# Performance work log

Measured on AMD Instinct MI355X. Metric: run time of the kernel, lower is better.

The kernel has to match this reference:

```python
import jax, jax.numpy as jnp
import numpy as np

N_WIRES = 12
BLOCK_CONFIGS = [(12, 3), (12, 3)]
HAM_OFFSET = 0.0
HAM_COEFF = 1.0
BATCH = 4096


def _sq(psi, w):
    # view statevector (B, 2^n) as (B, left, 2, right) isolating wire w
    B = psi.shape[0]
    n = N_WIRES
    return psi.reshape(B, 1 << w, 2, 1 << (n - 1 - w))


def _rx(psi, theta, w):
    s = _sq(psi, w)
    t = jnp.asarray(theta, jnp.float32).reshape(-1, 1, 1, 1) * 0.5
    out = jnp.cos(t) * s - 1j * jnp.sin(t) * jnp.flip(s, axis=2)
    return out.reshape(psi.shape)


def _ry(psi, theta, w):
    # [[c,-s],[s,c]]: new = cos*psi + sin*sgn*flip(psi), sgn = (-1, +1)
    s = _sq(psi, w)
    t = jnp.asarray(theta, jnp.float32).reshape(-1, 1, 1, 1) * 0.5
    sgn = jnp.array([-1.0, 1.0], jnp.float32).reshape(1, 1, 2, 1)
    out = jnp.cos(t) * s + jnp.sin(t) * sgn * jnp.flip(s, axis=2)
    return out.reshape(psi.shape)


def _rz(psi, theta, w):
    # diag(e^{-i t/2}, e^{+i t/2})
    s = _sq(psi, w)
    t = jnp.asarray(theta, jnp.float32).reshape(-1, 1, 1, 1) * 0.5
    z = jnp.array([-1.0, 1.0], jnp.float32).reshape(1, 1, 2, 1)
    out = s * jnp.exp(1j * (t * z).astype(jnp.complex64))
    return out.reshape(psi.shape)


def _cnot(psi, c, t):
    B = psi.shape[0]
    n = N_WIRES
    lo, hi = (c, t) if c < t else (t, c)
    s = psi.reshape(B, 1 << lo, 2, 1 << (hi - lo - 1), 2, 1 << (n - 1 - hi))
    ctrl_ax = 2 if c == lo else 4
    tgt_ax = 4 if c == lo else 2
    p0 = jax.lax.index_in_dim(s, 0, axis=ctrl_ax, keepdims=True)
    p1 = jnp.flip(jax.lax.index_in_dim(s, 1, axis=ctrl_ax, keepdims=True), axis=tgt_ax)
    out = jnp.concatenate([p0, p1], axis=ctrl_ax)
    return out.reshape(psi.shape)


def setup_inputs() -> dict:
    key = jax.random.key(0)
    k1, k2 = jax.random.split(key)
    total_encode = sum(ne for ne, _ in BLOCK_CONFIGS)
    total_ansatz = sum(ld for _, ld in BLOCK_CONFIGS)
    x = jax.random.normal(k1, (BATCH, total_encode), dtype=jnp.float32)
    ansatz_weights = jax.random.uniform(
        k2, (total_ansatz, 3, N_WIRES), dtype=jnp.float32,
        minval=-np.pi, maxval=np.pi)
    return {"x": x, "ansatz_weights": ansatz_weights}


def reference(x, ansatz_weights):
    B = x.shape[0]
    n = N_WIRES
    psi = jnp.zeros((B, 1 << n), jnp.complex64).at[:, 0].set(1.0)
    param_col = 0
    ansatz_block = 0
    for n_encode, linear_depth in BLOCK_CONFIGS:
        for j in range(n_encode):
            wire = j % n
            if param_col < x.shape[1]:
                psi = _rx(psi, x[:, param_col], wire)
            param_col += 1
        for _ in range(linear_depth):
            w = ansatz_weights[ansatz_block]
            for i in range(n):
                psi = _ry(psi, w[0, i], i)
                psi = _rz(psi, w[1, i], i)
                psi = _ry(psi, w[2, i], i)
            for i in range(n):
                psi = _cnot(psi, i, (i + 1) % n)
            ansatz_block += 1
    # <H> with H = offset + coeff * sum_i Z_i : diagonal = n - 2*popcount(k)
    probs = psi.real ** 2 + psi.imag ** 2
    k = jnp.arange(1 << n)
    pop = ((k[:, None] >> jnp.arange(n)[None, :]) & 1).sum(-1).astype(jnp.float32)
    diag = HAM_OFFSET + HAM_COEFF * (n - 2.0 * pop)
    expval = probs @ diag  # (B,)
    return expval[:, None]
```

## Files before the change

kernel.cpp:

```cpp
#include <hip/hip_runtime.h>
#include <math.h>

#define NTP 256
#define NT 64
#define NS 4096

typedef float f32x2 __attribute__((ext_vector_type(2)));

constexpr int ring_pi_c(int k) {
    int u = k ^ (k >> 1);
    u ^= u >> 2; u ^= u >> 4; u ^= u >> 8;
    int w0 = ((u >> 11) ^ u) & 1;
    return (u & 0x7FF) | (w0 << 11);
}
constexpr int gfun(int n) {
    int n0 = n & 1, n1 = (n >> 1) & 1, n2 = (n >> 2) & 1, n3 = (n >> 3) & 1;
    return (n1) | ((n0 ^ n1 ^ n2) << 1) | ((n0 ^ n2 ^ n3) << 2) | ((n0 ^ n3) << 3);
}
constexpr int sigf(int k) { return k ^ gfun((k >> 6) & 15); }

__device__ __forceinline__ void app1p(f32x2 ab, f32x2 cd, f32x2& a0, f32x2& a1) {
    f32x2 n0, n1;
    asm("v_pk_mul_f32 %0, %2, %4 op_sel:[0,0] op_sel_hi:[1,0]\n\t"
        "v_pk_fma_f32 %0, %2, %4, %0 op_sel:[1,1,0] op_sel_hi:[0,1,1] neg_hi:[0,1,0]\n\t"
        "v_pk_fma_f32 %0, %3, %5, %0 op_sel:[0,0,0] op_sel_hi:[1,0,1] neg_lo:[0,1,0] neg_hi:[0,1,0]\n\t"
        "v_pk_fma_f32 %0, %3, %5, %0 op_sel:[1,1,0] op_sel_hi:[0,1,1] neg_lo:[0,1,0]\n\t"
        "v_pk_mul_f32 %1, %3, %4 op_sel:[0,0] op_sel_hi:[1,0]\n\t"
        "v_pk_fma_f32 %1, %3, %4, %1 op_sel:[1,1,0] op_sel_hi:[0,1,1] neg_lo:[0,1,0]\n\t"
        "v_pk_fma_f32 %1, %2, %5, %1 op_sel:[0,0,0] op_sel_hi:[1,0,1]\n\t"
        "v_pk_fma_f32 %1, %2, %5, %1 op_sel:[1,1,0] op_sel_hi:[0,1,1] neg_lo:[0,1,0]"
        : "=&v"(n0), "=&v"(n1)
        : "v"(a0), "v"(a1), "v"(ab), "v"(cd));
    a0 = n0; a1 = n1;
}

template<int P>
__device__ __forceinline__ void gate_on_bit6(f32x2 a[64], f32x2 ab, f32x2 cd) {
    #pragma unroll
    for (int r = 0; r < 64; ++r)
        if (!(r & (1 << P)))
            app1p(ab, cd, a[r], a[r | (1 << P)]);
}

__device__ __forceinline__ void load_gate(const float4* __restrict__ Uw,
                                          const float2* __restrict__ cs12,
                                          int lay, int w, bool fold,
                                          f32x2& ab, f32x2& cd) {
    float4 g = Uw[lay * 12 + w];
    float A = g.x, B = g.y, C = g.z, D = g.w;
    if (fold) {
        float2 sc = cs12[w];
        float c = sc.x, s = sc.y;
        float A2 = A*c + D*s, B2 = B*c - C*s, C2 = C*c + B*s, D2 = D*c - A*s;
        A = A2; B = B2; C = C2; D = D2;
    }
    ab = f32x2{A, B}; cd = f32x2{C, D};
}

__global__ void prep_kernel(const float* __restrict__ x,
                            const float* __restrict__ wts,
                            float4* __restrict__ Uw,
                            float2* __restrict__ cs,
                            int total)
{
    int idx = blockIdx.x * blockDim.x + threadIdx.x;
    if (idx < total) {
        float th = 0.5f * x[idx];
        float s, c; sincosf(th, &s, &c);
        cs[idx] = make_float2(c, s);
    }
    if (idx < 72) {
        int ab = idx / 12, w = idx % 12;
        float a  = 0.5f * wts[(ab * 3 + 0) * 12 + w];
        float bb = 0.5f * wts[(ab * 3 + 1) * 12 + w];
        float g  = 0.5f * wts[(ab * 3 + 2) * 12 + w];
        float sa, ca, sb, cb, sg, cg;
        sincosf(a,  &sa, &ca);
        sincosf(bb, &sb, &cb);
        sincosf(g,  &sg, &cg);
        float A = cb * (ca * cg - sa * sg);
        float B = sb * (ca * cg + sa * sg);
        float C = cb * (sa * cg + ca * sg);
        float D = sb * (sa * cg - ca * sg);
        Uw[idx] = make_float4(A, B, C, D);
    }
}

__global__ __launch_bounds__(NT, 1)
void tqhea_kernel(const float4* __restrict__ Uw,
                  const float2* __restrict__ cs,
                  float* __restrict__ out)
{
    __shared__ f32x2 psi[NS];

    const int b  = blockIdx.x;
    const int ln = threadIdx.x;

    const float2* csb  = cs + b * 24;
    const float2* cs12 = csb + 12;

    f32x2 a[64];

    {
        float2 rc[12];
        #pragma unroll
        for (int i = 0; i < 12; ++i) rc[i] = csb[i];
        float mlan = 1.f;
        #pragma unroll
        for (int bit = 0; bit < 6; ++bit)
            mlan *= ((ln >> bit) & 1) ? rc[11 - bit].y : rc[11 - bit].x;
        int q = __popc(ln) & 3;
        float pre = (q == 0) ? mlan : (q == 2) ? -mlan : 0.f;
        float pim = (q == 1) ? -mlan : (q == 3) ? mlan : 0.f;
        float mA[8], mB[8];
        #pragma unroll
        for (int i = 0; i < 8; ++i) {
            mA[i] = (((i>>2)&1)?rc[0].y:rc[0].x) * (((i>>1)&1)?rc[1].y:rc[1].x) * ((i&1)?rc[2].y:rc[2].x);
            mB[i] = (((i>>2)&1)?rc[3].y:rc[3].x) * (((i>>1)&1)?rc[4].y:rc[4].x) * ((i&1)?rc[5].y:rc[5].x);
        }
        #pragma unroll
        for (int r = 0; r < 64; ++r) {
            float m = mA[r >> 3] * mB[r & 7];
            const int rot = __popc(r) & 3;
            float vx, vy;
            if (rot == 0)      { vx =  pre * m; vy =  pim * m; }
            else if (rot == 1) { vx =  pim * m; vy = -pre * m; }
            else if (rot == 2) { vx = -pre * m; vy = -pim * m; }
            else               { vx = -pim * m; vy =  pre * m; }
            a[r] = f32x2{vx, vy};
        }
    }

    const int gl    = gfun(ln & 15);
    const int baseB = (ln << 6) | gl;
    const int baseR = sigf(ring_pi_c(ln << 6));
    const int Pl    = ring_pi_c(ln << 6);

    float acc = 0.f;

    #pragma unroll 1
    for (int lay = 0; lay < 6; ++lay) {
        const bool fold = (lay == 3);
        f32x2 gab, gcd;

        load_gate(Uw, cs12, lay, 0, fold, gab, gcd); gate_on_bit6<5>(a, gab, gcd);
        load_gate(Uw, cs12, lay, 1, fold, gab, gcd); gate_on_bit6<4>(a, gab, gcd);
        load_gate(Uw, cs12, lay, 2, fold, gab, gcd); gate_on_bit6<3>(a, gab, gcd);
        load_gate(Uw, cs12, lay, 3, fold, gab, gcd); gate_on_bit6<2>(a, gab, gcd);
        load_gate(Uw, cs12, lay, 4, fold, gab, gcd); gate_on_bit6<1>(a, gab, gcd);
        load_gate(Uw, cs12, lay, 5, fold, gab, gcd); gate_on_bit6<0>(a, gab, gcd);

        #pragma unroll
        for (int r = 0; r < 64; ++r)
            psi[(r << 6) | (ln ^ gfun(r & 15))] = a[r];
        __syncthreads();
        #pragma unroll
        for (int r = 0; r < 64; ++r)
            a[r] = psi[(baseB ^ (r & 15)) | (r & 48)];

        load_gate(Uw, cs12, lay, 6,  fold, gab, gcd); gate_on_bit6<5>(a, gab, gcd);
        load_gate(Uw, cs12, lay, 7,  fold, gab, gcd); gate_on_bit6<4>(a, gab, gcd);
        load_gate(Uw, cs12, lay, 8,  fold, gab, gcd); gate_on_bit6<3>(a, gab, gcd);
        load_gate(Uw, cs12, lay, 9,  fold, gab, gcd); gate_on_bit6<2>(a, gab, gcd);
        load_gate(Uw, cs12, lay, 10, fold, gab, gcd); gate_on_bit6<1>(a, gab, gcd);
        load_gate(Uw, cs12, lay, 11, fold, gab, gcd); gate_on_bit6<0>(a, gab, gcd);

        if (lay < 5) {
            #pragma unroll
            for (int r = 0; r < 64; ++r)
                psi[baseR ^ sigf(ring_pi_c(r))] = a[r];
            __syncthreads();
            #pragma unroll
            for (int r = 0; r < 64; ++r)
                a[r] = psi[(r << 6) | (ln ^ gfun(r & 15))];
        } else {
            #pragma unroll
            for (int r = 0; r < 64; ++r) {
                float d = 12.0f - 2.0f * (float)__popc(Pl ^ ring_pi_c(r));
                acc += (a[r].x * a[r].x + a[r].y * a[r].y) * d;
            }
        }
    }

    #pragma unroll
    for (int off = 32; off > 0; off >>= 1)
        acc += __shfl_down(acc, off);
    if (ln == 0) out[b] = acc;
}

extern "C" void kernel_launch(void* const* d_in, const int* in_sizes, int n_in,
                              void* d_out, int out_size, void* d_ws, size_t ws_size,
                              hipStream_t stream) {
    const float* x   = (const float*)d_in[0];
    const float* wts = (const float*)d_in[1];
    float* out = (float*)d_out;
    int B = in_sizes[0] / 24;

    float4* Uw = (float4*)d_ws;
    float2* cs = (float2*)((char*)d_ws + 1152);
    int total = B * 24;

    prep_kernel<<<dim3((total + NTP - 1) / NTP), dim3(NTP), 0, stream>>>(x, wts, Uw, cs, total);
    tqhea_kernel<<<dim3(B), dim3(NT), 0, stream>>>(Uw, cs, out);
}
```

Measured before the change: 224.3 us.

## Process two batch samples per block, interleaving gate compute with LDS transposes

Each 64-thread block now simulates two statevectors, with the loop restructured into half-layer phases. Gate application on the second sample is scheduled between the shared-memory write and read of the first sample's transpose. This is meant to hide LDS transpose latency behind independent compute within a single wave. It doubles the register footprint per thread, which may cut waves per SIMD or cause spills, and it halves the grid size.

Result: slower. 339.2 us (+51.2%).

```diff
diff --git a/kernel.cpp b/kernel.cpp
--- a/kernel.cpp
+++ b/kernel.cpp
@@ -44,9 +44,9 @@
 
 __device__ __forceinline__ void load_gate(const float4* __restrict__ Uw,
                                           const float2* __restrict__ cs12,
-                                          int lay, int w, bool fold,
+                                          int gi, int w, bool fold,
                                           f32x2& ab, f32x2& cd) {
-    float4 g = Uw[lay * 12 + w];
+    float4 g = Uw[gi];
     float A = g.x, B = g.y, C = g.z, D = g.w;
     if (fold) {
         float2 sc = cs12[w];
@@ -55,6 +55,68 @@
         A = A2; B = B2; C = C2; D = D2;
     }
     ab = f32x2{A, B}; cd = f32x2{C, D};
+}
+
+__device__ __forceinline__ void gates6(f32x2 a[64], const float4* __restrict__ Uw,
+                                       const float2* __restrict__ cs12,
+                                       int lay, int half, bool fold) {
+    const int base = lay * 12 + half * 6, wb = half * 6;
+    f32x2 gab, gcd;
+    load_gate(Uw, cs12, base + 0, wb + 0, fold, gab, gcd); gate_on_bit6<5>(a, gab, gcd);
+    load_gate(Uw, cs12, base + 1, wb + 1, fold, gab, gcd); gate_on_bit6<4>(a, gab, gcd);
+    load_gate(Uw, cs12, base + 2, wb + 2, fold, gab, gcd); gate_on_bit6<3>(a, gab, gcd);
+    load_gate(Uw, cs12, base + 3, wb + 3, fold, gab, gcd); gate_on_bit6<2>(a, gab, gcd);
+    load_gate(Uw, cs12, base + 4, wb + 4, fold, gab, gcd); gate_on_bit6<1>(a, gab, gcd);
+    load_gate(Uw, cs12, base + 5, wb + 5, fold, gab, gcd); gate_on_bit6<0>(a, gab, gcd);
+}
+
+__device__ __forceinline__ void Twr(f32x2* psi, const f32x2 a[64], int ln, int baseR, bool ring) {
+    if (!ring) {
+        #pragma unroll
+        for (int r = 0; r < 64; ++r) psi[(r << 6) | (ln ^ gfun(r & 15))] = a[r];
+    } else {
+        #pragma unroll
+        for (int r = 0; r < 64; ++r) psi[baseR ^ sigf(ring_pi_c(r))] = a[r];
+    }
+}
+__device__ __forceinline__ void Trd(const f32x2* psi, f32x2 a[64], int ln, int baseB, bool ring) {
+    if (!ring) {
+        #pragma unroll
+        for (int r = 0; r < 64; ++r) a[r] = psi[(baseB ^ (r & 15)) | (r & 48)];
+    } else {
+        #pragma unroll
+        for (int r = 0; r < 64; ++r) a[r] = psi[(r << 6) | (ln ^ gfun(r & 15))];
+    }
+}
+
+__device__ __forceinline__ void init_state(f32x2 a[64], const float2* __restrict__ csb, int ln) {
+    float2 rc[12];
+    #pragma unroll
+    for (int i = 0; i < 12; ++i) rc[i] = csb[i];
+    float mlan = 1.f;
+    #pragma unroll
+    for (int bit = 0; bit < 6; ++bit)
+        mlan *= ((ln >> bit) & 1) ? rc[11 - bit].y : rc[11 - bit].x;
+    int q = __popc(ln) & 3;
+    float pre = (q == 0) ? mlan : (q == 2) ? -mlan : 0.f;
+    float pim = (q == 1) ? -mlan : (q == 3) ? mlan : 0.f;
+    float mA[8], mB[8];
+    #pragma unroll
+    for (int i = 0; i < 8; ++i) {
+        mA[i] = (((i>>2)&1)?rc[0].y:rc[0].x) * (((i>>1)&1)?rc[1].y:rc[1].x) * ((i&1)?rc[2].y:rc[2].x);
+        mB[i] = (((i>>2)&1)?rc[3].y:rc[3].x) * (((i>>1)&1)?rc[4].y:rc[4].x) * ((i&1)?rc[5].y:rc[5].x);
+    }
+    #pragma unroll
+    for (int r = 0; r < 64; ++r) {
+        float m = mA[r >> 3] * mB[r & 7];
+        const int rot = __popc(r) & 3;
+        float vx, vy;
+        if (rot == 0)      { vx =  pre * m; vy =  pim * m; }
+        else if (rot == 1) { vx =  pim * m; vy = -pre * m; }
+        else if (rot == 2) { vx = -pre * m; vy = -pim * m; }
+        else               { vx = -pim * m; vy =  pre * m; }
+        a[r] = f32x2{vx, vy};
+    }
 }
 
 __global__ void prep_kernel(const float* __restrict__ x,
@@ -93,99 +155,58 @@
 {
     __shared__ f32x2 psi[NS];
 
-    const int b  = blockIdx.x;
-    const int ln = threadIdx.x;
-
-    const float2* csb  = cs + b * 24;
-    const float2* cs12 = csb + 12;
-
-    f32x2 a[64];
-
-    {
-        float2 rc[12];
-        #pragma unroll
-        for (int i = 0; i < 12; ++i) rc[i] = csb[i];
-        float mlan = 1.f;
-        #pragma unroll
-        for (int bit = 0; bit < 6; ++bit)
-            mlan *= ((ln >> bit) & 1) ? rc[11 - bit].y : rc[11 - bit].x;
-        int q = __popc(ln) & 3;
-        float pre = (q == 0) ? mlan : (q == 2) ? -mlan : 0.f;
-        float pim = (q == 1) ? -mlan : (q == 3) ? mlan : 0.f;
-        float mA[8], mB[8];
-        #pragma unroll
-        for (int i = 0; i < 8; ++i) {
-            mA[i] = (((i>>2)&1)?rc[0].y:rc[0].x) * (((i>>1)&1)?rc[1].y:rc[1].x) * ((i&1)?rc[2].y:rc[2].x);
-            mB[i] = (((i>>2)&1)?rc[3].y:rc[3].x) * (((i>>1)&1)?rc[4].y:rc[4].x) * ((i&1)?rc[5].y:rc[5].x);
-        }
-        #pragma unroll
-        for (int r = 0; r < 64; ++r) {
-            float m = mA[r >> 3] * mB[r & 7];
-            const int rot = __popc(r) & 3;
-            float vx, vy;
-            if (rot == 0)      { vx =  pre * m; vy =  pim * m; }
-            else if (rot == 1) { vx =  pim * m; vy = -pre * m; }
-            else if (rot == 2) { vx = -pre * m; vy = -pim * m; }
-            else               { vx = -pim * m; vy =  pre * m; }
-            a[r] = f32x2{vx, vy};
-        }
-    }
+    const int ln  = threadIdx.x;
+    const int b0  = blockIdx.x << 1;
+    const int b1  = b0 | 1;
+
+    const float2* cs0  = cs + b0 * 24;
+    const float2* cs1  = cs + b1 * 24;
+    const float2* cs12_0 = cs0 + 12;
+    const float2* cs12_1 = cs1 + 12;
+
+    f32x2 aa[64], ab[64];
+    init_state(aa, cs0, ln);
+    init_state(ab, cs1, ln);
 
     const int gl    = gfun(ln & 15);
     const int baseB = (ln << 6) | gl;
     const int baseR = sigf(ring_pi_c(ln << 6));
-    const int Pl    = ring_pi_c(ln << 6);
-
-    float acc = 0.f;
 
     #pragma unroll 1
-    for (int lay = 0; lay < 6; ++lay) {
+    for (int p = 0; p < 11; ++p) {
+        const int lay = p >> 1, half = p & 1;
         const bool fold = (lay == 3);
-        f32x2 gab, gcd;
-
-        load_gate(Uw, cs12, lay, 0, fold, gab, gcd); gate_on_bit6<5>(a, gab, gcd);
-        load_gate(Uw, cs12, lay, 1, fold, gab, gcd); gate_on_bit6<4>(a, gab, gcd);
-        load_gate(Uw, cs12, lay, 2, fold, gab, gcd); gate_on_bit6<3>(a, gab, gcd);
-        load_gate(Uw, cs12, lay, 3, fold, gab, gcd); gate_on_bit6<2>(a, gab, gcd);
-        load_gate(Uw, cs12, lay, 4, fold, gab, gcd); gate_on_bit6<1>(a, gab, gcd);
-        load_gate(Uw, cs12, lay, 5, fold, gab, gcd); gate_on_bit6<0>(a, gab, gcd);
-
-        #pragma unroll
-        for (int r = 0; r < 64; ++r)
-            psi[(r << 6) | (ln ^ gfun(r & 15))] = a[r];
-        __syncthreads();
-        #pragma unroll
-        for (int r = 0; r < 64; ++r)
-            a[r] = psi[(baseB ^ (r & 15)) | (r & 48)];
-
-        load_gate(Uw, cs12, lay, 6,  fold, gab, gcd); gate_on_bit6<5>(a, gab, gcd);
-        load_gate(Uw, cs12, lay, 7,  fold, gab, gcd); gate_on_bit6<4>(a, gab, gcd);
-        load_gate(Uw, cs12, lay, 8,  fold, gab, gcd); gate_on_bit6<3>(a, gab, gcd);
-        load_gate(Uw, cs12, lay, 9,  fold, gab, gcd); gate_on_bit6<2>(a, gab, gcd);
-        load_gate(Uw, cs12, lay, 10, fold, gab, gcd); gate_on_bit6<1>(a, gab, gcd);
-        load_gate(Uw, cs12, lay, 11, fold, gab, gcd); gate_on_bit6<0>(a, gab, gcd);
-
-        if (lay < 5) {
-            #pragma unroll
-            for (int r = 0; r < 64; ++r)
-                psi[baseR ^ sigf(ring_pi_c(r))] = a[r];
-            __syncthreads();
-            #pragma unroll
-            for (int r = 0; r < 64; ++r)
-                a[r] = psi[(r << 6) | (ln ^ gfun(r & 15))];
-        } else {
-            #pragma unroll
-            for (int r = 0; r < 64; ++r) {
-                float d = 12.0f - 2.0f * (float)__popc(Pl ^ ring_pi_c(r));
-                acc += (a[r].x * a[r].x + a[r].y * a[r].y) * d;
-            }
-        }
-    }
-
-    #pragma unroll
-    for (int off = 32; off > 0; off >>= 1)
-        acc += __shfl_down(acc, off);
-    if (ln == 0) out[b] = acc;
+        const bool ring = (half == 1);
+
+        gates6(aa, Uw, cs12_0, lay, half, fold);
+        __syncthreads();
+        Twr(psi, aa, ln, baseR, ring);
+        gates6(ab, Uw, cs12_1, lay, half, fold);
+        __syncthreads();
+        Trd(psi, aa, ln, baseB, ring);
+        __syncthreads();
+        Twr(psi, ab, ln, baseR, ring);
+        __syncthreads();
+        Trd(psi, ab, ln, baseB, ring);
+    }
+
+    gates6(aa, Uw, cs12_0, 5, 1, false);
+    gates6(ab, Uw, cs12_1, 5, 1, false);
+
+    const int Pl = ring_pi_c(ln << 6);
+    float acc0 = 0.f, acc1 = 0.f;
+    #pragma unroll
+    for (int r = 0; r < 64; ++r) {
+        float d = 12.0f - 2.0f * (float)__popc(Pl ^ ring_pi_c(r));
+        acc0 += (aa[r].x * aa[r].x + aa[r].y * aa[r].y) * d;
+        acc1 += (ab[r].x * ab[r].x + ab[r].y * ab[r].y) * d;
+    }
+    #pragma unroll
+    for (int off = 32; off > 0; off >>= 1) {
+        acc0 += __shfl_down(acc0, off);
+        acc1 += __shfl_down(acc1, off);
+    }
+    if (ln == 0) { out[b0] = acc0; out[b1] = acc1; }
 }
 
 extern "C" void kernel_launch(void* const* d_in, const int* in_sizes, int n_in,
@@ -201,5 +222,5 @@
     int total = B * 24;
 
     prep_kernel<<<dim3((total + NTP - 1) / NTP), dim3(NTP), 0, stream>>>(x, wts, Uw, cs, total);
-    tqhea_kernel<<<dim3(B), dim3(NT), 0, stream>>>(Uw, cs, out);
-}
+    tqhea_kernel<<<dim3(B / 2), dim3(NT), 0, stream>>>(Uw, cs, out);
+}
```
